# Kernel tuning notes

Hardware: AMD Instinct MI355X
Metric: run time of the kernel (lower is better)

Reference implementation:

```python
import jax, jax.numpy as jnp
import numpy as np

B, T, D, H = 4, 2048, 1024, 16
HD = D // H  # head_dim = 64

def setup_inputs() -> dict:
    key = jax.random.key(0)
    k1, k2, k3 = jax.random.split(key, 3)
    scale_in = 1.0 / np.sqrt(D)
    return {
        "x": jax.random.normal(k1, (B, T, D), dtype=jnp.float32),
        "W_qkv": jax.random.normal(k2, (D, 3 * D), dtype=jnp.float32) * scale_in,
        "b_qkv": jnp.zeros((3 * D,), dtype=jnp.float32),
        "W_out": jax.random.normal(k3, (D, D), dtype=jnp.float32) * scale_in,
        "b_out": jnp.zeros((D,), dtype=jnp.float32),
    }

def reference(x, W_qkv, b_qkv, W_out, b_out):
    Bx, Tx, C = x.shape
    qkv = x @ W_qkv + b_qkv                      # [B,T,3D]
    q, k, v = jnp.split(qkv, 3, axis=-1)
    # [B,T,D] -> [B,H,T,hd]
    def to_heads(t):
        return t.reshape(Bx, Tx, H, HD).transpose(0, 2, 1, 3)
    q, k, v = to_heads(q), to_heads(k), to_heads(v)
    scores = jnp.einsum('bhqd,bhkd->bhqk', q, k) / np.sqrt(HD)  # [B,H,T,T]
    causal = jnp.tril(jnp.ones((Tx, Tx), dtype=bool))
    scores = jnp.where(causal, scores, -jnp.inf)
    attn = jax.nn.softmax(scores, axis=-1)       # dropout p=0 -> identity
    out = jnp.einsum('bhqk,bhkd->bhqd', attn, v)  # [B,H,T,hd]
    out = out.transpose(0, 2, 1, 3).reshape(Bx, Tx, C)
    return out @ W_out + b_out
```

## Files before the change

### kernel.cpp

```cpp
#include <hip/hip_runtime.h>
#include <hip/hip_bf16.h>

#define BB 4
#define TT 2048
#define DD 1024
#define HH 16
#define HDIM 64
#define BT (BB*TT)
#define D3 (3*DD)

typedef __attribute__((ext_vector_type(8))) short bf16x8;
typedef __attribute__((ext_vector_type(4))) float f32x4;

#if __has_builtin(__builtin_amdgcn_exp2f)
#define EXP2(x) __builtin_amdgcn_exp2f(x)
#else
#define EXP2(x) exp2f(x)
#endif

__device__ __forceinline__ ushort f2bf(float f) {
  union { float f; uint32_t u; } v; v.f = f;
  uint32_t u = v.u + 0x7FFFu + ((v.u >> 16) & 1u);
  return (ushort)(u >> 16);
}

__device__ __forceinline__ ushort f2bf_hw(float f) {
  __hip_bfloat16 h = __float2bfloat16(f);
  ushort u;
  __builtin_memcpy(&u, &h, 2);
  return u;
}

__device__ __forceinline__ float bf2f(ushort u) {
  union { uint32_t i; float f; } x; x.i = ((uint32_t)u) << 16; return x.f;
}

__device__ __forceinline__ void gload_lds16(const void* g, void* l) {
  __builtin_amdgcn_global_load_lds((const __attribute__((address_space(1))) void*)g,
                                   (__attribute__((address_space(3))) void*)l, 16, 0, 0);
}

__global__ __launch_bounds__(256)
void cvt_bf16(const float* __restrict__ in, ushort* __restrict__ out, int n4,
              uint* __restrict__ ctr) {
  if (blockIdx.x == 0 && threadIdx.x == 0) *ctr = 0u;
  int i = blockIdx.x * blockDim.x + threadIdx.x;
  int stride = gridDim.x * blockDim.x;
  for (; i < n4; i += stride) {
    float4 v = ((const float4*)in)[i];
    ushort4 o;
    o.x = f2bf(v.x); o.y = f2bf(v.y); o.z = f2bf(v.z); o.w = f2bf(v.w);
    ((ushort4*)out)[i] = o;
  }
}

__global__ __launch_bounds__(256)
void transpose_cvt2(const float* __restrict__ Wq, ushort* __restrict__ Wtq,
                    const float* __restrict__ Wo, ushort* __restrict__ Wto) {
  const int flat = blockIdx.x;
  const bool isQ = flat < 48 * 16;
  const int lx = isQ ? flat : flat - 48 * 16;
  const int N = isQ ? D3 : DD;
  const int nb = N / 64;
  const float* W = isQ ? Wq : Wo;
  ushort* Wt = isQ ? Wtq : Wto;
  const int n0 = (lx % nb) * 64;
  const int k0 = (lx / nb) * 64;

  __shared__ ushort Tt[64][68];
  const int tid = threadIdx.x;
  const int r = tid >> 4;
  const int c4 = (tid & 15) * 4;
  #pragma unroll
  for (int i = 0; i < 4; ++i) {
    int row = r + i * 16;
    float4 v = *(const float4*)&W[(size_t)(k0 + row) * N + n0 + c4];
    Tt[c4 + 0][row] = f2bf(v.x);
    Tt[c4 + 1][row] = f2bf(v.y);
    Tt[c4 + 2][row] = f2bf(v.z);
    Tt[c4 + 3][row] = f2bf(v.w);
  }
  __syncthreads();
  #pragma unroll
  for (int i = 0; i < 4; ++i) {
    int row = r + i * 16;
    ushort4 tv = *(const ushort4*)&Tt[row][c4];
    *(ushort4*)&Wt[(size_t)(n0 + row) * 1024 + k0 + c4] = tv;
  }
}

template<bool F32OUT>
__global__ __launch_bounds__(512, 2)
void gemm_8p(const ushort* __restrict__ A, const ushort* __restrict__ Bw,
             const float* __restrict__ bias, void* __restrict__ C, int N) {
  __shared__ __align__(16) short lds[2 * (128 + 256) * 64];

  const int tid = threadIdx.x;
  const int w = tid >> 6;
  const int wm = w >> 2;
  const int wn = w & 3;
  const int lane = tid & 63;
  const int li = lane & 15, g = lane >> 4;
  const int swz = (li & 7) << 4;

  const int bm = blockIdx.y * 128;
  const int bn = blockIdx.x * 256;
  const ushort* Ag = A + (size_t)bm * 1024;
  const ushort* Bg = Bw + (size_t)bn * 1024;

  const int lrow8 = lane >> 3;
  const int chsw = (lane & 7) ^ lrow8;

  f32x4 acc[4][4] = {};

#define STAGE6(t, p) do { \
  const int kk_ = (t) * 64; \
  short* Ad_ = lds + (p) * 24576; \
  short* Bd_ = Ad_ + 8192; \
  _Pragma("unroll") \
  for (int h_ = 0; h_ < 2; ++h_) { \
    const int r_ = h_ * 64 + w * 8; \
    gload_lds16(Ag + (size_t)(r_ + lrow8) * 1024 + kk_ + chsw * 8, Ad_ + r_ * 64); \
  } \
  _Pragma("unroll") \
  for (int j_ = 0; j_ < 4; ++j_) { \
    const int r_ = j_ * 64 + w * 8; \
    gload_lds16(Bg + (size_t)(r_ + lrow8) * 1024 + kk_ + chsw * 8, Bd_ + r_ * 64); \
  } \
} while (0)

  STAGE6(0, 0);
  asm volatile("s_waitcnt vmcnt(0)" ::: "memory");
  __builtin_amdgcn_sched_barrier(0);
  __builtin_amdgcn_s_barrier();

  for (int s = 0; s < 16; ++s) {
    const int cur = s & 1;
    const char* Ab = (const char*)lds + cur * 49152;
    const char* Bb = Ab + 16384;

    if (s + 1 < 16) STAGE6(s + 1, cur ^ 1);

    #pragma unroll
    for (int kh = 0; kh < 2; ++kh) {
      bf16x8 af[4], bf[4];
      #pragma unroll
      for (int mi = 0; mi < 4; ++mi)
        af[mi] = *(const bf16x8*)(Ab + (wm * 64 + mi * 16 + li) * 128 + ((kh * 64 + g * 16) ^ swz));
      #pragma unroll
      for (int ni = 0; ni < 4; ++ni)
        bf[ni] = *(const bf16x8*)(Bb + (wn * 64 + ni * 16 + li) * 128 + ((kh * 64 + g * 16) ^ swz));
      __builtin_amdgcn_s_setprio(1);
      #pragma unroll
      for (int mi = 0; mi < 4; ++mi)
        #pragma unroll
        for (int ni = 0; ni < 4; ++ni)
          acc[mi][ni] = __builtin_amdgcn_mfma_f32_16x16x32_bf16(af[mi], bf[ni], acc[mi][ni], 0, 0, 0);
      __builtin_amdgcn_s_setprio(0);
      if (kh == 0) __builtin_amdgcn_s_barrier();
    }
    asm volatile("s_waitcnt vmcnt(0)" ::: "memory");
    __builtin_amdgcn_sched_barrier(0);
    __builtin_amdgcn_s_barrier();
  }
#undef STAGE6

  #pragma unroll
  for (int ni = 0; ni < 4; ++ni) {
    int col = bn + wn * 64 + ni * 16 + li;
    float bv = bias[col];
    #pragma unroll
    for (int mi = 0; mi < 4; ++mi) {
      int row = bm + wm * 64 + mi * 16 + g * 4;
      #pragma unroll
      for (int r = 0; r < 4; ++r) {
        float v = acc[mi][ni][r] + bv;
        if (F32OUT) ((float*)C)[(size_t)(row + r) * N + col] = v;
        else        ((ushort*)C)[(size_t)(row + r) * N + col] = f2bf_hw(v);
      }
    }
  }
}

#define NITEMS 1024

__global__ __launch_bounds__(256)
void attn_mfma(const ushort* __restrict__ qkv, ushort* __restrict__ out,
               uint* __restrict__ ctr) {
  __shared__ __align__(16) short Ks[64 * 64];
  __shared__ __align__(16) short Vt[64 * 64];
  __shared__ __align__(16) short Pl[4 * 16 * 64];
  __shared__ int s_item;

  const int tid = threadIdx.x;
  const int w = tid >> 6;
  const int lane = tid & 63;
  const int li = lane & 15, g = lane >> 4;
  const int sw = (li & 7) << 4;

  char* KsB = (char*)Ks;
  char* VtB = (char*)Vt;
  char* PlB = (char*)Pl + w * 2048;

  const int krow0 = tid >> 3;
  const int kc = tid & 7;
  const int d0 = (tid >> 5) * 8;
  const int kp = tid & 31;
  const int kswz = (kc * 16) ^ ((krow0 & 7) << 4);

  for (;;) {
    if (tid == 0) s_item = (int)atomicAdd(ctr, 1u);
    __syncthreads();
    const int item = s_item;
    if (item >= NITEMS) return;

    const int qt = 15 - (item >> 6);
    const int bh = item & 63;
    const int h = bh & 15, b = bh >> 4;
    const int qg0 = qt * 128 + w * 32;

    bf16x8 qfr[2][2];
    #pragma unroll
    for (int qf = 0; qf < 2; ++qf) {
      const ushort* qrow = qkv + (size_t)(b * TT + qg0 + qf * 16 + li) * D3 + h * HDIM;
      #pragma unroll
      for (int c = 0; c < 2; ++c) {
        uint4 raw = *(const uint4*)(qrow + c * 32 + g * 8);
        const ushort* rp = (const ushort*)&raw;
        bf16x8 v;
        #pragma unroll
        for (int j = 0; j < 8; ++j)
          v[j] = (short)f2bf_hw(bf2f(rp[j]) * 0.18033688f);
        qfr[qf][c] = v;
      }
    }

    f32x4 o[4][2] = {};
    float lsum[2] = {0.f, 0.f};

    const ushort* kbase = qkv + (size_t)b * TT * D3 + DD + h * HDIM;
    const ushort* vbase = kbase + DD;

    const int nt = 2 * qt + 2;
    const int itlast = 2 * qt + (w >> 1);

    uint4 kpre0, kpre1, vpre0, vpre1;
    {
      const ushort* kg = kbase + (size_t)krow0 * D3 + kc * 8;
      kpre0 = *(const uint4*)kg;
      kpre1 = *(const uint4*)(kg + (size_t)32 * D3);
      const ushort* vg = vbase + (size_t)(2 * kp) * D3 + d0;
      vpre0 = *(const uint4*)vg;
      vpre1 = *(const uint4*)(vg + D3);
    }

    for (int it = 0; it < nt; ++it) {
      const int k0 = it * 64;
      *(uint4*)(KsB + krow0 * 128 + kswz) = kpre0;
      *(uint4*)(KsB + (krow0 + 32) * 128 + kswz) = kpre1;
      {
        const ushort* pa = (const ushort*)&vpre0;
        const ushort* pb = (const ushort*)&vpre1;
        #pragma unroll
        for (int j = 0; j < 8; ++j) {
          uint32_t pk = (uint32_t)pa[j] | ((uint32_t)pb[j] << 16);
          *(uint32_t*)(VtB + (d0 + j) * 128 + ((4 * kp) ^ (j << 4))) = pk;
        }
      }
      __syncthreads();
      if (it + 1 < nt) {
        const ushort* kg = kbase + (size_t)(k0 + 64 + krow0) * D3 + kc * 8;
        kpre0 = *(const uint4*)kg;
        kpre1 = *(const uint4*)(kg + (size_t)32 * D3);
        const ushort* vg = vbase + (size_t)(k0 + 64 + 2 * kp) * D3 + d0;
        vpre0 = *(const uint4*)vg;
        vpre1 = *(const uint4*)(vg + D3);
      }
      if (it <= itlast) {
        const bool domask = (it == itlast);
        bf16x8 pf[2][2];
        f32x4 s[2][4];
        __builtin_amdgcn_s_setprio(1);
        #pragma unroll
        for (int kt = 0; kt < 4; ++kt) {
          const int row = kt * 16 + li;
          bf16x8 kf0 = *(bf16x8*)(KsB + row * 128 + ((g * 16) ^ sw));
          bf16x8 kf1 = *(bf16x8*)(KsB + row * 128 + ((64 + g * 16) ^ sw));
          #pragma unroll
          for (int qf = 0; qf < 2; ++qf) {
            f32x4 a = {0.f, 0.f, 0.f, 0.f};
            a = __builtin_amdgcn_mfma_f32_16x16x32_bf16(kf0, qfr[qf][0], a, 0, 0, 0);
            a = __builtin_amdgcn_mfma_f32_16x16x32_bf16(kf1, qfr[qf][1], a, 0, 0, 0);
            s[qf][kt] = a;
          }
        }
        __builtin_amdgcn_s_setprio(0);
        #pragma unroll
        for (int qf = 0; qf < 2; ++qf) {
          const int qrow = qg0 + qf * 16 + li;
          if (domask) {
            #pragma unroll
            for (int kt = 0; kt < 4; ++kt)
              #pragma unroll
              for (int r = 0; r < 4; ++r) {
                int key = k0 + kt * 16 + g * 4 + r;
                if (key > qrow) s[qf][kt][r] = -1e30f;
              }
          }
          float ls = 0.f;
          #pragma unroll
          for (int kt = 0; kt < 4; ++kt) {
            float p0 = EXP2(s[qf][kt][0]);
            float p1 = EXP2(s[qf][kt][1]);
            float p2 = EXP2(s[qf][kt][2]);
            float p3 = EXP2(s[qf][kt][3]);
            ls += (p0 + p1) + (p2 + p3);
            uint2 val;
            val.x = (uint32_t)f2bf_hw(p0) | ((uint32_t)f2bf_hw(p1) << 16);
            val.y = (uint32_t)f2bf_hw(p2) | ((uint32_t)f2bf_hw(p3) << 16);
            *(uint2*)(PlB + li * 128 + ((kt * 32 + g * 8) ^ sw)) = val;
          }
          lsum[qf] += ls;
          pf[qf][0] = *(bf16x8*)(PlB + li * 128 + ((g * 16) ^ sw));
          pf[qf][1] = *(bf16x8*)(PlB + li * 128 + ((64 + g * 16) ^ sw));
        }
        __builtin_amdgcn_s_setprio(1);
        #pragma unroll
        for (int dt = 0; dt < 4; ++dt) {
          const int vrow = dt * 16 + li;
          bf16x8 vf0 = *(bf16x8*)(VtB + vrow * 128 + ((g * 16) ^ sw));
          bf16x8 vf1 = *(bf16x8*)(VtB + vrow * 128 + ((64 + g * 16) ^ sw));
          #pragma unroll
          for (int qf = 0; qf < 2; ++qf) {
            o[dt][qf] = __builtin_amdgcn_mfma_f32_16x16x32_bf16(vf0, pf[qf][0], o[dt][qf], 0, 0, 0);
            o[dt][qf] = __builtin_amdgcn_mfma_f32_16x16x32_bf16(vf1, pf[qf][1], o[dt][qf], 0, 0, 0);
          }
        }
        __builtin_amdgcn_s_setprio(0);
      }
      __syncthreads();
    }

    #pragma unroll
    for (int qf = 0; qf < 2; ++qf) {
      float lt = lsum[qf];
      lt += __shfl_xor(lt, 16);
      lt += __shfl_xor(lt, 32);
      float inv = 1.f / lt;
      ushort* orow = out + (size_t)(b * TT + qg0 + qf * 16 + li) * DD + h * HDIM;
      #pragma unroll
      for (int dt = 0; dt < 4; ++dt) {
        uint2 pk;
        pk.x = (uint32_t)f2bf_hw(o[dt][qf][0] * inv) | ((uint32_t)f2bf_hw(o[dt][qf][1] * inv) << 16);
        pk.y = (uint32_t)f2bf_hw(o[dt][qf][2] * inv) | ((uint32_t)f2bf_hw(o[dt][qf][3] * inv) << 16);
        *(uint2*)&orow[dt * 16 + g * 4] = pk;
      }
    }
  }
}

extern "C" void kernel_launch(void* const* d_in, const int* in_sizes, int n_in,
                              void* d_out, int out_size, void* d_ws, size_t ws_size,
                              hipStream_t stream) {
  const float* x     = (const float*)d_in[0];
  const float* W_qkv = (const float*)d_in[1];
  const float* b_qkv = (const float*)d_in[2];
  const float* W_out = (const float*)d_in[3];
  const float* b_out = (const float*)d_in[4];
  float* out = (float*)d_out;

  ushort* x_bf   = (ushort*)d_ws;
  ushort* wtq    = x_bf + (size_t)BT * DD;
  ushort* wto    = wtq + (size_t)D3 * DD;
  ushort* qkv_bf = wto + (size_t)DD * DD;
  ushort* att_bf = qkv_bf + (size_t)BT * D3;
  uint*   ctr    = (uint*)(att_bf + (size_t)BT * DD);

  cvt_bf16<<<2048, 256, 0, stream>>>(x, x_bf, BT * DD / 4, ctr);
  transpose_cvt2<<<dim3(48 * 16 + 16 * 16), 256, 0, stream>>>(W_qkv, wtq, W_out, wto);

  gemm_8p<false><<<dim3(D3 / 256, BT / 128), 512, 0, stream>>>(x_bf, wtq, b_qkv, (void*)qkv_bf, D3);
  attn_mfma<<<dim3(1024), 256, 0, stream>>>(qkv_bf, att_bf, ctr);
  gemm_8p<true><<<dim3(DD / 256, BT / 128), 512, 0, stream>>>(att_bf, wto, b_out, (void*)out, DD);
}
```

Before: 178.3 us.

## Stage two K/V tiles per barrier pair in attention loop

The attention loop now loads and stages 128 keys (two 64-key tiles) into doubled K and V shared-memory buffers per iteration, then processes both tiles between one pair of barriers. This halves the number of __syncthreads per work item and issues twice as many global prefetch loads at once, so more memory latency can overlap with compute. The cost is more LDS (about 16KB more), more prefetch registers, and an extra barrier on the work-item fetch, because the item slot now lives in the P buffer. This may lower occupancy.

```diff
diff --git a/kernel.cpp b/kernel.cpp
--- a/kernel.cpp
+++ b/kernel.cpp
@@ -187,10 +187,11 @@
 __global__ __launch_bounds__(256)
 void attn_mfma(const ushort* __restrict__ qkv, ushort* __restrict__ out,
                uint* __restrict__ ctr) {
-  __shared__ __align__(16) short Ks[64 * 64];
-  __shared__ __align__(16) short Vt[64 * 64];
+  __shared__ __align__(16) short Ks[2][64 * 64];
+  __shared__ __align__(16) short Vt[2][64 * 64];
   __shared__ __align__(16) short Pl[4 * 16 * 64];
-  __shared__ int s_item;
+
+  volatile int* s_item = (volatile int*)&Pl[0];
 
   const int tid = threadIdx.x;
   const int w = tid >> 6;
@@ -198,8 +199,6 @@
   const int li = lane & 15, g = lane >> 4;
   const int sw = (li & 7) << 4;
 
-  char* KsB = (char*)Ks;
-  char* VtB = (char*)Vt;
   char* PlB = (char*)Pl + w * 2048;
 
   const int krow0 = tid >> 3;
@@ -209,9 +208,10 @@
   const int kswz = (kc * 16) ^ ((krow0 & 7) << 4);
 
   for (;;) {
-    if (tid == 0) s_item = (int)atomicAdd(ctr, 1u);
+    if (tid == 0) *s_item = (int)atomicAdd(ctr, 1u);
     __syncthreads();
-    const int item = s_item;
+    const int item = *s_item;
+    __syncthreads();
     if (item >= NITEMS) return;
 
     const int qt = 15 - (item >> 6);
@@ -241,102 +241,126 @@
     const ushort* kbase = qkv + (size_t)b * TT * D3 + DD + h * HDIM;
     const ushort* vbase = kbase + DD;
 
-    const int nt = 2 * qt + 2;
+    const int nw = qt + 1;
     const int itlast = 2 * qt + (w >> 1);
 
-    uint4 kpre0, kpre1, vpre0, vpre1;
+    uint4 kpre0, kpre1, kpre2, kpre3, vpre0, vpre1, vpre2, vpre3;
     {
       const ushort* kg = kbase + (size_t)krow0 * D3 + kc * 8;
       kpre0 = *(const uint4*)kg;
       kpre1 = *(const uint4*)(kg + (size_t)32 * D3);
+      kpre2 = *(const uint4*)(kg + (size_t)64 * D3);
+      kpre3 = *(const uint4*)(kg + (size_t)96 * D3);
       const ushort* vg = vbase + (size_t)(2 * kp) * D3 + d0;
       vpre0 = *(const uint4*)vg;
       vpre1 = *(const uint4*)(vg + D3);
-    }
-
-    for (int it = 0; it < nt; ++it) {
-      const int k0 = it * 64;
-      *(uint4*)(KsB + krow0 * 128 + kswz) = kpre0;
-      *(uint4*)(KsB + (krow0 + 32) * 128 + kswz) = kpre1;
+      vpre2 = *(const uint4*)(vg + (size_t)64 * D3);
+      vpre3 = *(const uint4*)(vg + (size_t)65 * D3);
+    }
+
+    for (int it = 0; it < nw; ++it) {
       {
+        char* Ks0 = (char*)Ks[0];
+        char* Ks1 = (char*)Ks[1];
+        *(uint4*)(Ks0 + krow0 * 128 + kswz) = kpre0;
+        *(uint4*)(Ks0 + (krow0 + 32) * 128 + kswz) = kpre1;
+        *(uint4*)(Ks1 + krow0 * 128 + kswz) = kpre2;
+        *(uint4*)(Ks1 + (krow0 + 32) * 128 + kswz) = kpre3;
+        char* Vt0 = (char*)Vt[0];
+        char* Vt1 = (char*)Vt[1];
         const ushort* pa = (const ushort*)&vpre0;
         const ushort* pb = (const ushort*)&vpre1;
+        const ushort* pc = (const ushort*)&vpre2;
+        const ushort* pd = (const ushort*)&vpre3;
         #pragma unroll
         for (int j = 0; j < 8; ++j) {
-          uint32_t pk = (uint32_t)pa[j] | ((uint32_t)pb[j] << 16);
-          *(uint32_t*)(VtB + (d0 + j) * 128 + ((4 * kp) ^ (j << 4))) = pk;
+          uint32_t pk0 = (uint32_t)pa[j] | ((uint32_t)pb[j] << 16);
+          uint32_t pk1 = (uint32_t)pc[j] | ((uint32_t)pd[j] << 16);
+          *(uint32_t*)(Vt0 + (d0 + j) * 128 + ((4 * kp) ^ (j << 4))) = pk0;
+          *(uint32_t*)(Vt1 + (d0 + j) * 128 + ((4 * kp) ^ (j << 4))) = pk1;
         }
       }
       __syncthreads();
-      if (it + 1 < nt) {
-        const ushort* kg = kbase + (size_t)(k0 + 64 + krow0) * D3 + kc * 8;
+      if (it + 1 < nw) {
+        const ushort* kg = kbase + (size_t)((it + 1) * 128 + krow0) * D3 + kc * 8;
         kpre0 = *(const uint4*)kg;
         kpre1 = *(const uint4*)(kg + (size_t)32 * D3);
-        const ushort* vg = vbase + (size_t)(k0 + 64 + 2 * kp) * D3 + d0;
+        kpre2 = *(const uint4*)(kg + (size_t)64 * D3);
+        kpre3 = *(const uint4*)(kg + (size_t)96 * D3);
+        const ushort* vg = vbase + (size_t)((it + 1) * 128 + 2 * kp) * D3 + d0;
         vpre0 = *(const uint4*)vg;
         vpre1 = *(const uint4*)(vg + D3);
-      }
-      if (it <= itlast) {
-        const bool domask = (it == itlast);
-        bf16x8 pf[2][2];
-        f32x4 s[2][4];
-        __builtin_amdgcn_s_setprio(1);
-        #pragma unroll
-        for (int kt = 0; kt < 4; ++kt) {
-          const int row = kt * 16 + li;
-          bf16x8 kf0 = *(bf16x8*)(KsB + row * 128 + ((g * 16) ^ sw));
-          bf16x8 kf1 = *(bf16x8*)(KsB + row * 128 + ((64 + g * 16) ^ sw));
+        vpre2 = *(const uint4*)(vg + (size_t)64 * D3);
+        vpre3 = *(const uint4*)(vg + (size_t)65 * D3);
+      }
+      #pragma unroll
+      for (int c = 0; c < 2; ++c) {
+        const int t = 2 * it + c;
+        if (t <= itlast) {
+          const bool domask = (t == itlast);
+          const int k0 = t * 64;
+          const char* KsB = (const char*)Ks[c];
+          const char* VtB = (const char*)Vt[c];
+          bf16x8 pf[2][2];
+          f32x4 s[2][4];
+          __builtin_amdgcn_s_setprio(1);
+          #pragma unroll
+          for (int kt = 0; kt < 4; ++kt) {
+            const int row = kt * 16 + li;
+            bf16x8 kf0 = *(bf16x8*)(KsB + row * 128 + ((g * 16) ^ sw));
+            bf16x8 kf1 = *(bf16x8*)(KsB + row * 128 + ((64 + g * 16) ^ sw));
+            #pragma unroll
+            for (int qf = 0; qf < 2; ++qf) {
+              f32x4 a = {0.f, 0.f, 0.f, 0.f};
+              a = __builtin_amdgcn_mfma_f32_16x16x32_bf16(kf0, qfr[qf][0], a, 0, 0, 0);
+              a = __builtin_amdgcn_mfma_f32_16x16x32_bf16(kf1, qfr[qf][1], a, 0, 0, 0);
+              s[qf][kt] = a;
+            }
+          }
+          __builtin_amdgcn_s_setprio(0);
           #pragma unroll
           for (int qf = 0; qf < 2; ++qf) {
-            f32x4 a = {0.f, 0.f, 0.f, 0.f};
-            a = __builtin_amdgcn_mfma_f32_16x16x32_bf16(kf0, qfr[qf][0], a, 0, 0, 0);
-            a = __builtin_amdgcn_mfma_f32_16x16x32_bf16(kf1, qfr[qf][1], a, 0, 0, 0);
-            s[qf][kt] = a;
+            const int qrow = qg0 + qf * 16 + li;
+            if (domask) {
+              #pragma unroll
+              for (int kt = 0; kt < 4; ++kt)
+                #pragma unroll
+                for (int r = 0; r < 4; ++r) {
+                  int key = k0 + kt * 16 + g * 4 + r;
+                  if (key > qrow) s[qf][kt][r] = -1e30f;
+                }
+            }
+            float ls = 0.f;
+            #pragma unroll
+            for (int kt = 0; kt < 4; ++kt) {
+              float p0 = EXP2(s[qf][kt][0]);
+              float p1 = EXP2(s[qf][kt][1]);
+              float p2 = EXP2(s[qf][kt][2]);
+              float p3 = EXP2(s[qf][kt][3]);
+              ls += (p0 + p1) + (p2 + p3);
+              uint2 val;
+              val.x = (uint32_t)f2bf_hw(p0) | ((uint32_t)f2bf_hw(p1) << 16);
+              val.y = (uint32_t)f2bf_hw(p2) | ((uint32_t)f2bf_hw(p3) << 16);
+              *(uint2*)(PlB + li * 128 + ((kt * 32 + g * 8) ^ sw)) = val;
+            }
+            lsum[qf] += ls;
+            pf[qf][0] = *(bf16x8*)(PlB + li * 128 + ((g * 16) ^ sw));
+            pf[qf][1] = *(bf16x8*)(PlB + li * 128 + ((64 + g * 16) ^ sw));
           }
+          __builtin_amdgcn_s_setprio(1);
+          #pragma unroll
+          for (int dt = 0; dt < 4; ++dt) {
+            const int vrow = dt * 16 + li;
+            bf16x8 vf0 = *(bf16x8*)(VtB + vrow * 128 + ((g * 16) ^ sw));
+            bf16x8 vf1 = *(bf16x8*)(VtB + vrow * 128 + ((64 + g * 16) ^ sw));
+            #pragma unroll
+            for (int qf = 0; qf < 2; ++qf) {
+              o[dt][qf] = __builtin_amdgcn_mfma_f32_16x16x32_bf16(vf0, pf[qf][0], o[dt][qf], 0, 0, 0);
+              o[dt][qf] = __builtin_amdgcn_mfma_f32_16x16x32_bf16(vf1, pf[qf][1], o[dt][qf], 0, 0, 0);
+            }
+          }
+          __builtin_amdgcn_s_setprio(0);
         }
-        __builtin_amdgcn_s_setprio(0);
-        #pragma unroll
-        for (int qf = 0; qf < 2; ++qf) {
-          const int qrow = qg0 + qf * 16 + li;
-          if (domask) {
-            #pragma unroll
-            for (int kt = 0; kt < 4; ++kt)
-              #pragma unroll
-              for (int r = 0; r < 4; ++r) {
-                int key = k0 + kt * 16 + g * 4 + r;
-                if (key > qrow) s[qf][kt][r] = -1e30f;
-              }
-          }
-          float ls = 0.f;
-          #pragma unroll
-          for (int kt = 0; kt < 4; ++kt) {
-            float p0 = EXP2(s[qf][kt][0]);
-            float p1 = EXP2(s[qf][kt][1]);
-            float p2 = EXP2(s[qf][kt][2]);
-            float p3 = EXP2(s[qf][kt][3]);
-            ls += (p0 + p1) + (p2 + p3);
-            uint2 val;
-            val.x = (uint32_t)f2bf_hw(p0) | ((uint32_t)f2bf_hw(p1) << 16);
-            val.y = (uint32_t)f2bf_hw(p2) | ((uint32_t)f2bf_hw(p3) << 16);
-            *(uint2*)(PlB + li * 128 + ((kt * 32 + g * 8) ^ sw)) = val;
-          }
-          lsum[qf] += ls;
-          pf[qf][0] = *(bf16x8*)(PlB + li * 128 + ((g * 16) ^ sw));
-          pf[qf][1] = *(bf16x8*)(PlB + li * 128 + ((64 + g * 16) ^ sw));
-        }
-        __builtin_amdgcn_s_setprio(1);
-        #pragma unroll
-        for (int dt = 0; dt < 4; ++dt) {
-          const int vrow = dt * 16 + li;
-          bf16x8 vf0 = *(bf16x8*)(VtB + vrow * 128 + ((g * 16) ^ sw));
-          bf16x8 vf1 = *(bf16x8*)(VtB + vrow * 128 + ((64 + g * 16) ^ sw));
-          #pragma unroll
-          for (int qf = 0; qf < 2; ++qf) {
-            o[dt][qf] = __builtin_amdgcn_mfma_f32_16x16x32_bf16(vf0, pf[qf][0], o[dt][qf], 0, 0, 0);
-            o[dt][qf] = __builtin_amdgcn_mfma_f32_16x16x32_bf16(vf1, pf[qf][1], o[dt][qf], 0, 0, 0);
-          }
-        }
-        __builtin_amdgcn_s_setprio(0);
       }
       __syncthreads();
     }
```

Result: no change. 180.1 us (+1.0%).
